# Kernel optimization log

Hardware: AMD Instinct MI355X
Metric: run time of the kernel (lower is better)

## Reference

```python
import jax, jax.numpy as jnp
import numpy as np

SPLIT_SHAPE = (16, 16, 16, 16)  # per-variable state counts; joint space = 65536
NUM_CLASSES = 100
STABLE = 1e-6


def setup_inputs() -> dict:
    key = jax.random.key(0)
    k1, k2 = jax.random.split(key)
    B = 1024
    logits = jax.random.normal(k1, (B, sum(SPLIT_SHAPE)), dtype=jnp.float32)
    labels = jax.random.randint(k2, (B,), 0, NUM_CLASSES)
    y_true = jax.nn.one_hot(labels, NUM_CLASSES, dtype=jnp.float32)
    return {"logits": logits, "y_true": y_true}


def reference(logits, y_true):
    B = logits.shape[0]
    # split logits into per-variable blocks and softmax each -> P(Ak|Xi)
    splits = np.cumsum(SPLIT_SHAPE)[:-1]
    variables = [jax.nn.softmax(p, axis=-1) for p in jnp.split(logits, splits, axis=-1)]
    # joint sample space via iterative outer products: [B, s1, ..., sN]
    joint = variables[0]
    for v in variables[1:]:
        joint = jnp.einsum('b...,ba->b...a', joint, v)
    flat = joint.reshape(B, -1)  # [B, J], J = prod(SPLIT_SHAPE)
    # observation: numerator/denominator counts (fresh recorder, first call)
    num_y_joint = jnp.einsum('bj,by->yj', flat, y_true)  # [Y, J]
    num_joint = jnp.sum(flat, axis=0)                     # [J]
    prob_y_joint = jnp.clip(
        jnp.maximum(num_y_joint, STABLE) / jnp.maximum(num_joint, STABLE), 0.0, 1.0)
    # inference: posterior P^A(Yi|Xi)
    probs = jnp.einsum('yj,bj->by', prob_y_joint, flat)  # [B, Y]
    return probs
```

## Files before the change

kernel.cpp:

```cpp
#include <hip/hip_runtime.h>
#include <hip/hip_bf16.h>

#define EPS 1e-6f

typedef float f32x4 __attribute__((ext_vector_type(4)));
typedef __bf16 bf16x8 __attribute__((ext_vector_type(8)));
typedef short short8 __attribute__((ext_vector_type(8)));

static __device__ __forceinline__ short bf16bits(float x) {
    __hip_bfloat16 h = __float2bfloat16(x);
    short s;
    __builtin_memcpy(&s, &h, 2);
    return s;
}
static __device__ __forceinline__ void bsplit(float x, short& h, short& l) {
    __hip_bfloat16 hb = __float2bfloat16(x);
    __builtin_memcpy(&h, &hb, 2);
    float hf = __bfloat162float(hb);
    __hip_bfloat16 lb = __float2bfloat16(x - hf);
    __builtin_memcpy(&l, &lb, 2);
}

static __device__ __forceinline__ bf16x8 gload16(const short* p) {
    bf16x8 r;
    asm volatile("global_load_dwordx4 %0, %1, off"
                 : "=&v"(r) : "v"(p) : "memory");
    return r;
}
#define WAITV(N)                                                   \
    do {                                                           \
        asm volatile("s_waitcnt vmcnt(" #N ")" ::: "memory");      \
        __builtin_amdgcn_sched_barrier(0);                         \
    } while (0)

__global__ __launch_bounds__(256) void kA(const float* __restrict__ logits,
                                          const float* __restrict__ y_true,
                                          float* __restrict__ P23,
                                          float* __restrict__ P01,
                                          float* __restrict__ P01T,
                                          short* __restrict__ P23s_hi,
                                          int* __restrict__ label,
                                          float* __restrict__ numjoint) {
    __shared__ float row[64];
    int b = blockIdx.x, t = threadIdx.x;
    if (t < 64) {
        float x = logits[b * 64 + t];
        float m = x;
        for (int mk = 8; mk >= 1; mk >>= 1) m = fmaxf(m, __shfl_xor(m, mk, 16));
        float e = __expf(x - m);
        float s = e;
        for (int mk = 8; mk >= 1; mk >>= 1) s += __shfl_xor(s, mk, 16);
        row[t] = e / s;
    }
    if (t >= 128 && t < 228) {
        int y = t - 128;
        if (y_true[b * 100 + y] > 0.5f) label[b] = y;
    }
    if (t < 64) numjoint[b * 64 + t] = 0.f;
    __syncthreads();
    int hi = t >> 4, lo = t & 15;
    float v01 = row[hi] * row[16 + lo];
    float v23 = row[32 + hi] * row[48 + lo];
    P01[b * 256 + t] = v01;
    P01T[t * 1024 + b] = v01;
    P23[b * 256 + t] = v23;
    int ts = t ^ ((b & 7) << 3);
    P23s_hi[b * 256 + ts] = bf16bits(v23);
}

__global__ __launch_bounds__(256, 4) void kSNJ(const float* __restrict__ P01T,
                                               const float* __restrict__ P23,
                                               const int* __restrict__ label,
                                               int* __restrict__ bidx,
                                               int* __restrict__ off_g,
                                               float* __restrict__ numjoint) {
    int t = threadIdx.x;
    int bid = blockIdx.x;

    if (bid == 512) {
        __shared__ int lab[1024];
        __shared__ unsigned bm[101 * 32];
        __shared__ int hist[101];
        __shared__ int offs[101];
        for (int i = t; i < 1024; i += 256) lab[i] = label[i];
        if (t < 101) hist[t] = 0;
        for (int i = t; i < 101 * 32; i += 256) bm[i] = 0u;
        __syncthreads();
        for (int i = t; i < 1024; i += 256) {
            int my = lab[i];
            atomicAdd(&hist[my], 1);
            atomicOr(&bm[my * 32 + (i >> 5)], 1u << (i & 31));
        }
        __syncthreads();
        if (t == 0) {
            int s = 0;
            for (int y = 0; y < 101; ++y) { offs[y] = s; s += hist[y]; }
        }
        __syncthreads();
        for (int i = t; i < 1024; i += 256) {
            int my = lab[i];
            int w = i >> 5;
            int rank = 0;
            for (int q = 0; q < 32; ++q)
                if (q < w) rank += __popc(bm[my * 32 + q]);
            rank += __popc(bm[my * 32 + w] & ((1u << (i & 31)) - 1u));
            bidx[offs[my] + rank] = i;
        }
        if (t <= 100) off_g[t] = offs[t];
        return;
    }

    __shared__ short Bh[4 * 64 * 8];
    __shared__ short Bl[4 * 64 * 8];
    int ub = (bid & 3) << 6;
    int tb = ((bid >> 2) & 3) << 6;
    int koff = (bid >> 4) << 5;
    int lane = t & 63, w = t >> 6;
    int l15 = lane & 15, l4 = lane >> 4;

    const float* pa = P01T + (size_t)(ub + w * 16 + l15) * 1024 + koff + (l4 << 3);
    int sr = t >> 3, sc = (t & 7) << 3;

    const f32x4 zero4 = {0.f, 0.f, 0.f, 0.f};
    f32x4 acc0 = zero4, acc1 = zero4, acc2 = zero4, acc3 = zero4;

    {
        const float* pb = P23 + (size_t)(koff + sr) * 256 + tb + sc;
        #pragma unroll
        for (int q = 0; q < 8; ++q) {
            short h, l;
            bsplit(pb[q], h, l);
            int tcl = sc + q;
            int ad = (((tcl >> 4) << 6) + (tcl & 15) + ((sr >> 3) << 4)) * 8 + (sr & 7);
            Bh[ad] = h; Bl[ad] = l;
        }
    }
    __syncthreads();
    union { short8 s; bf16x8 b; } Ah, Al;
    #pragma unroll
    for (int q = 0; q < 8; ++q) {
        short h, l;
        bsplit(pa[q], h, l);
        Ah.s[q] = h; Al.s[q] = l;
    }
    {
        bf16x8 bh0 = *(const bf16x8*)(Bh + (lane) * 8);
        bf16x8 bl0 = *(const bf16x8*)(Bl + (lane) * 8);
        bf16x8 bh1 = *(const bf16x8*)(Bh + (64 + lane) * 8);
        bf16x8 bl1 = *(const bf16x8*)(Bl + (64 + lane) * 8);
        bf16x8 bh2 = *(const bf16x8*)(Bh + (128 + lane) * 8);
        bf16x8 bl2 = *(const bf16x8*)(Bl + (128 + lane) * 8);
        bf16x8 bh3 = *(const bf16x8*)(Bh + (192 + lane) * 8);
        bf16x8 bl3 = *(const bf16x8*)(Bl + (192 + lane) * 8);
        acc0 = __builtin_amdgcn_mfma_f32_16x16x32_bf16(Ah.b, bh0, acc0, 0, 0, 0);
        acc0 = __builtin_amdgcn_mfma_f32_16x16x32_bf16(Ah.b, bl0, acc0, 0, 0, 0);
        acc0 = __builtin_amdgcn_mfma_f32_16x16x32_bf16(Al.b, bh0, acc0, 0, 0, 0);
        acc1 = __builtin_amdgcn_mfma_f32_16x16x32_bf16(Ah.b, bh1, acc1, 0, 0, 0);
        acc1 = __builtin_amdgcn_mfma_f32_16x16x32_bf16(Ah.b, bl1, acc1, 0, 0, 0);
        acc1 = __builtin_amdgcn_mfma_f32_16x16x32_bf16(Al.b, bh1, acc1, 0, 0, 0);
        acc2 = __builtin_amdgcn_mfma_f32_16x16x32_bf16(Ah.b, bh2, acc2, 0, 0, 0);
        acc2 = __builtin_amdgcn_mfma_f32_16x16x32_bf16(Ah.b, bl2, acc2, 0, 0, 0);
        acc2 = __builtin_amdgcn_mfma_f32_16x16x32_bf16(Al.b, bh2, acc2, 0, 0, 0);
        acc3 = __builtin_amdgcn_mfma_f32_16x16x32_bf16(Ah.b, bh3, acc3, 0, 0, 0);
        acc3 = __builtin_amdgcn_mfma_f32_16x16x32_bf16(Ah.b, bl3, acc3, 0, 0, 0);
        acc3 = __builtin_amdgcn_mfma_f32_16x16x32_bf16(Al.b, bh3, acc3, 0, 0, 0);
    }
    #pragma unroll
    for (int n = 0; n < 4; ++n) {
        f32x4 a = (n == 0) ? acc0 : (n == 1) ? acc1 : (n == 2) ? acc2 : acc3;
        #pragma unroll
        for (int r = 0; r < 4; ++r) {
            int u = ub + w * 16 + (l4 << 2) + r;
            int tc = tb + (n << 4) + l15;
            atomicAdd(&numjoint[u * 256 + tc], a[r]);
        }
    }
}

__global__ __launch_bounds__(256, 2) void kY(const float* __restrict__ P01,
                                             const float* __restrict__ P23,
                                             const int* __restrict__ bidx,
                                             const int* __restrict__ off_g,
                                             const float* __restrict__ numjoint,
                                             short* __restrict__ pyF) {
    __shared__ short Bh[4 * 64 * 8];
    __shared__ short Bl[4 * 64 * 8];
    __shared__ short ct[4][16 * 64];
    __shared__ float aStage[32][258];
    __shared__ int sbidx[32];
    int y = blockIdx.x >> 2;
    int qd = blockIdx.x & 3;
    int t = threadIdx.x;
    int lane = t & 63, w = t >> 6;
    int l15 = lane & 15, l4 = lane >> 4;
    int yt = y >> 4, yl = y & 15;

    if (y >= 100) {
        short8 z = {0, 0, 0, 0, 0, 0, 0, 0};
        #pragma unroll
        for (int ut = 0; ut < 4; ++ut)
            #pragma unroll
            for (int rep = 0; rep < 2; ++rep) {
                int c = (rep << 6) + lane;
                int ul = c >> 3, t8 = (c & 7) << 3;
                int u = (w << 6) + (ut << 4) + ul;
                int j0 = u * 256 + (qd << 6) + t8;
                size_t sa = ((size_t)((j0 >> 5) * 8 + yt) * 64 + yl + (((j0 >> 3) & 3) << 4)) * 8;
                *(short8*)(pyF + sa) = z;
            }
        return;
    }

    int off = off_g[y];
    int n = off_g[y + 1] - off;
    int nk = (n + 31) >> 5;

    const f32x4 zero4 = {0.f, 0.f, 0.f, 0.f};
    f32x4 acc[4][4];
    #pragma unroll
    for (int a = 0; a < 4; ++a)
        #pragma unroll
        for (int b = 0; b < 4; ++b) acc[a][b] = zero4;

    int sr = t >> 3, sc = (t & 7) << 3;

    #pragma unroll 1
    for (int kc = 0; kc < nk; ++kc) {
        __syncthreads();
        if (t < 32) {
            int idx = off + kc * 32 + t;
            sbidx[t] = bidx[(idx < 1024) ? idx : 1023];
        }
        __syncthreads();
        for (int it = 0; it < 32; ++it)
            aStage[it][t] = P01[sbidx[it] * 256 + t];
        {
            int row = kc * 32 + sr;
            float vals[8];
            if (row < n) {
                const float* pb = P23 + (size_t)sbidx[sr] * 256 + (qd << 6) + sc;
                #pragma unroll
                for (int q = 0; q < 8; ++q) vals[q] = pb[q];
            } else {
                #pragma unroll
                for (int q = 0; q < 8; ++q) vals[q] = 0.f;
            }
            #pragma unroll
            for (int q = 0; q < 8; ++q) {
                short h, l;
                bsplit(vals[q], h, l);
                int tl = sc + q;
                int ad = (((tl >> 4) << 6) + (tl & 15) + ((sr >> 3) << 4)) * 8 + (sr & 7);
                Bh[ad] = h; Bl[ad] = l;
            }
        }
        __syncthreads();
        #pragma unroll
        for (int ut = 0; ut < 4; ++ut) {
            union { short8 s; bf16x8 b; } Ah, Al;
            #pragma unroll
            for (int q = 0; q < 8; ++q) {
                short h, l;
                bsplit(aStage[(l4 << 3) + q][(w << 6) + (ut << 4) + l15], h, l);
                Ah.s[q] = h; Al.s[q] = l;
            }
            #pragma unroll
            for (int tt = 0; tt < 4; ++tt) {
                bf16x8 bh = *(const bf16x8*)(Bh + ((tt << 6) + lane) * 8);
                bf16x8 bl = *(const bf16x8*)(Bl + ((tt << 6) + lane) * 8);
                acc[ut][tt] = __builtin_amdgcn_mfma_f32_16x16x32_bf16(Ah.b, bh, acc[ut][tt], 0, 0, 0);
                acc[ut][tt] = __builtin_amdgcn_mfma_f32_16x16x32_bf16(Ah.b, bl, acc[ut][tt], 0, 0, 0);
                acc[ut][tt] = __builtin_amdgcn_mfma_f32_16x16x32_bf16(Al.b, bh, acc[ut][tt], 0, 0, 0);
            }
        }
    }

    #pragma unroll
    for (int ut = 0; ut < 4; ++ut) {
        #pragma unroll
        for (int tt = 0; tt < 4; ++tt) {
            #pragma unroll
            for (int r = 0; r < 4; ++r) {
                int u = (w << 6) + (ut << 4) + (l4 << 2) + r;
                int tg = (qd << 6) + (tt << 4) + l15;
                float nj = numjoint[u * 256 + tg];
                float q = fminf(fmaxf(acc[ut][tt][r], EPS) / fmaxf(nj, EPS), 1.0f);
                ct[w][((l4 << 2) + r) * 64 + (tt << 4) + l15] = bf16bits(q);
            }
        }
        asm volatile("s_waitcnt lgkmcnt(0)" ::: "memory");
        __builtin_amdgcn_sched_barrier(0);
        #pragma unroll
        for (int rep = 0; rep < 2; ++rep) {
            int c = (rep << 6) + lane;
            int ul = c >> 3, t8 = (c & 7) << 3;
            short8 v = *(const short8*)(ct[w] + ul * 64 + t8);
            int u = (w << 6) + (ut << 4) + ul;
            int j0 = u * 256 + (qd << 6) + t8;
            size_t sa = ((size_t)((j0 >> 5) * 8 + yt) * 64 + yl + (((j0 >> 3) & 3) << 4)) * 8;
            *(short8*)(pyF + sa) = v;
        }
        asm volatile("s_waitcnt lgkmcnt(0)" ::: "memory");
        __builtin_amdgcn_sched_barrier(0);
    }
}

__global__ __launch_bounds__(256, 3) void kC(const short* __restrict__ P23s_hi,
                                             const float* __restrict__ P01T,
                                             const short* __restrict__ pyF,
                                             float* __restrict__ part) {
    __shared__ short Ahi[64 * 256];
    __shared__ float p01s[512];
    int t = threadIdx.x;
    int bb = blockIdx.x >> 5, uspl = blockIdx.x & 31;
    int bbase = bb << 6;
    int u0 = uspl << 3;

    #pragma unroll
    for (int r = 0; r < 8; ++r) {
        int c = r * 256 + t;
        *(short8*)(Ahi + c * 8) = *(const short8*)(P23s_hi + bbase * 256 + c * 8);
    }
    p01s[t] = P01T[(u0 + (t >> 6)) * 1024 + bbase + (t & 63)];
    p01s[256 + t] = P01T[(u0 + 4 + (t >> 6)) * 1024 + bbase + (t & 63)];
    __syncthreads();

    int lane = t & 63;
    int wy = t >> 6;
    int l15 = lane & 15, l4 = lane >> 4;
    int hi8 = l4 << 3;

    int swz = (l15 & 7) << 3;
    const short* pA0h = Ahi + l15 * 256;
    const short* pA1h = pA0h + 16 * 256;
    const short* pA2h = pA0h + 32 * 256;
    const short* pA3h = pA0h + 48 * 256;

    const short* pf = pyF + (size_t)(uspl * 512 + wy * 2) * 512 + lane * 8;
    int y0 = wy * 32 + l15;

    const f32x4 zero4 = {0.f, 0.f, 0.f, 0.f};
    f32x4 P00 = zero4, P01v = zero4, P10 = zero4, P11 = zero4;
    f32x4 P20 = zero4, P21 = zero4, P30 = zero4, P31 = zero4;
    bf16x8 W0, W1, X0, X1, Y0, Y1, Z0, Z1;

#define COMPUTE(CUR0, CUR1, KS)                                                  \
    {                                                                            \
        int aoff = ((KS) * 32 + hi8) ^ swz;                                      \
        bf16x8 a0h = *(const bf16x8*)(pA0h + aoff);                              \
        bf16x8 a1h = *(const bf16x8*)(pA1h + aoff);                              \
        bf16x8 a2h = *(const bf16x8*)(pA2h + aoff);                              \
        bf16x8 a3h = *(const bf16x8*)(pA3h + aoff);                              \
        f32x4 c00 = ((KS) == 0) ? zero4 : Q00;                                   \
        f32x4 c01 = ((KS) == 0) ? zero4 : Q01;                                   \
        f32x4 c10 = ((KS) == 0) ? zero4 : Q10;                                   \
        f32x4 c11 = ((KS) == 0) ? zero4 : Q11;                                   \
        f32x4 c20 = ((KS) == 0) ? zero4 : Q20;                                   \
        f32x4 c21 = ((KS) == 0) ? zero4 : Q21;                                   \
        f32x4 c30 = ((KS) == 0) ? zero4 : Q30;                                   \
        f32x4 c31 = ((KS) == 0) ? zero4 : Q31;                                   \
        c00 = __builtin_amdgcn_mfma_f32_16x16x32_bf16(a0h, CUR0, c00, 0, 0, 0);  \
        c10 = __builtin_amdgcn_mfma_f32_16x16x32_bf16(a1h, CUR0, c10, 0, 0, 0);  \
        c20 = __builtin_amdgcn_mfma_f32_16x16x32_bf16(a2h, CUR0, c20, 0, 0, 0);  \
        c30 = __builtin_amdgcn_mfma_f32_16x16x32_bf16(a3h, CUR0, c30, 0, 0, 0);  \
        c01 = __builtin_amdgcn_mfma_f32_16x16x32_bf16(a0h, CUR1, c01, 0, 0, 0);  \
        c11 = __builtin_amdgcn_mfma_f32_16x16x32_bf16(a1h, CUR1, c11, 0, 0, 0);  \
        c21 = __builtin_amdgcn_mfma_f32_16x16x32_bf16(a2h, CUR1, c21, 0, 0, 0);  \
        c31 = __builtin_amdgcn_mfma_f32_16x16x32_bf16(a3h, CUR1, c31, 0, 0, 0);  \
        Q00 = c00; Q01 = c01; Q10 = c10; Q11 = c11;                              \
        Q20 = c20; Q21 = c21; Q30 = c30; Q31 = c31;                              \
    }
#define STEP(CUR0, CUR1, NXT0, NXT1, KS, S3)    \
    NXT0 = gload16(pf + (S3) * 4096);           \
    NXT1 = gload16(pf + (S3) * 4096 + 512);     \
    WAITV(6);                                   \
    COMPUTE(CUR0, CUR1, KS)

    {
        W0 = gload16(pf);        W1 = gload16(pf + 512);
        X0 = gload16(pf + 4096); X1 = gload16(pf + 4096 + 512);
        Y0 = gload16(pf + 8192); Y1 = gload16(pf + 8192 + 512);
    }

    #pragma unroll 1
    for (int uu = 0; uu < 7; ++uu) {
        int s0 = uu * 8;
        f32x4 Q00, Q01, Q10, Q11, Q20, Q21, Q30, Q31;
        STEP(W0, W1, Z0, Z1, 0, s0 + 3)
        STEP(X0, X1, W0, W1, 1, s0 + 4)
        STEP(Y0, Y1, X0, X1, 2, s0 + 5)
        STEP(Z0, Z1, Y0, Y1, 3, s0 + 6)
        STEP(W0, W1, Z0, Z1, 4, s0 + 7)
        STEP(X0, X1, W0, W1, 5, s0 + 8)
        STEP(Y0, Y1, X0, X1, 6, s0 + 9)
        STEP(Z0, Z1, Y0, Y1, 7, s0 + 10)
        f32x4 pv0 = *(const f32x4*)(p01s + uu * 64 + (l4 << 2));
        f32x4 pv1 = *(const f32x4*)(p01s + uu * 64 + 16 + (l4 << 2));
        f32x4 pv2 = *(const f32x4*)(p01s + uu * 64 + 32 + (l4 << 2));
        f32x4 pv3 = *(const f32x4*)(p01s + uu * 64 + 48 + (l4 << 2));
        P00 += pv0 * Q00; P01v += pv0 * Q01;
        P10 += pv1 * Q10; P11 += pv1 * Q11;
        P20 += pv2 * Q20; P21 += pv2 * Q21;
        P30 += pv3 * Q30; P31 += pv3 * Q31;
    }
    {
        f32x4 Q00, Q01, Q10, Q11, Q20, Q21, Q30, Q31;
        STEP(W0, W1, Z0, Z1, 0, 59)
        STEP(X0, X1, W0, W1, 1, 60)
        STEP(Y0, Y1, X0, X1, 2, 61)
        STEP(Z0, Z1, Y0, Y1, 3, 62)
        STEP(W0, W1, Z0, Z1, 4, 63)
        WAITV(4); COMPUTE(X0, X1, 5)
        WAITV(2); COMPUTE(Y0, Y1, 6)
        WAITV(0); COMPUTE(Z0, Z1, 7)
        f32x4 pv0 = *(const f32x4*)(p01s + 7 * 64 + (l4 << 2));
        f32x4 pv1 = *(const f32x4*)(p01s + 7 * 64 + 16 + (l4 << 2));
        f32x4 pv2 = *(const f32x4*)(p01s + 7 * 64 + 32 + (l4 << 2));
        f32x4 pv3 = *(const f32x4*)(p01s + 7 * 64 + 48 + (l4 << 2));
        P00 += pv0 * Q00; P01v += pv0 * Q01;
        P10 += pv1 * Q10; P11 += pv1 * Q11;
        P20 += pv2 * Q20; P21 += pv2 * Q21;
        P30 += pv3 * Q30; P31 += pv3 * Q31;
    }
#undef STEP
#undef COMPUTE

    size_t pbase = (size_t)uspl * 128 * 1024;
    {
        int bg0 = bbase + (l4 << 2);
        size_t r0 = pbase + (size_t)y0 * 1024;
        size_t r1 = pbase + (size_t)(y0 + 16) * 1024;
        *(f32x4*)(part + r0 + bg0)      = P00;
        *(f32x4*)(part + r0 + bg0 + 16) = P10;
        *(f32x4*)(part + r0 + bg0 + 32) = P20;
        *(f32x4*)(part + r0 + bg0 + 48) = P30;
        *(f32x4*)(part + r1 + bg0)      = P01v;
        *(f32x4*)(part + r1 + bg0 + 16) = P11;
        *(f32x4*)(part + r1 + bg0 + 32) = P21;
        *(f32x4*)(part + r1 + bg0 + 48) = P31;
    }
}

__global__ __launch_bounds__(256) void kD(const float* __restrict__ part,
                                          float* __restrict__ out) {
    int t = threadIdx.x;
    int y = blockIdx.x >> 2;
    int b = ((blockIdx.x & 3) << 8) + t;
    float s = 0.f;
    for (int q = 0; q < 32; ++q)
        s += part[(((size_t)q * 128 + y) << 10) + b];
    out[(size_t)b * 100 + y] = s;
}

extern "C" void kernel_launch(void* const* d_in, const int* in_sizes, int n_in,
                              void* d_out, int out_size, void* d_ws, size_t ws_size,
                              hipStream_t stream) {
    const float* logits = (const float*)d_in[0];
    const float* y_true = (const float*)d_in[1];
    float* out = (float*)d_out;

    char* ws = (char*)d_ws;
    float* P01      = (float*)(ws);
    float* P23      = (float*)(ws + (1u << 20));
    float* P01T     = (float*)(ws + (2u << 20));
    short* P23s_hi  = (short*)(ws + (3u << 20));
    int*   lab      = (int*)(ws + (4u << 20));
    int*   bidx     = (int*)(ws + (4u << 20) + 4096);
    int*   off_g    = (int*)(ws + (4u << 20) + 8192);
    short* pyF      = (short*)(ws + (8u << 20));
    float* numjoint = (float*)(ws + (24u << 20));
    float* part     = (float*)(ws + (40u << 20));

    kA<<<1024, 256, 0, stream>>>(logits, y_true, P23, P01, P01T, P23s_hi, lab, numjoint);
    kSNJ<<<513, 256, 0, stream>>>(P01T, P23, lab, bidx, off_g, numjoint);
    kY<<<512, 256, 0, stream>>>(P01, P23, bidx, off_g, numjoint, pyF);
    kC<<<512, 256, 0, stream>>>(P23s_hi, P01T, pyF, part);
    kD<<<400, 256, 0, stream>>>(part, out);
}
```

Measured before the change: 67.03 us.

## Fuse split-K reduction into kC via last-block atomic counter

Removes the separate kD reduction launch. Each kC block bumps a per-batch-tile atomic counter after writing its partials, and the last of the 32 u-split blocks for that tile sums the partials and writes the output. The counter is reset in kA. This saves one kernel launch and its dependency gap, but leaves the reduction to only 16 blocks running serially at the tail of kC, with threadfence overhead added to every block.

```diff
diff --git a/kernel.cpp b/kernel.cpp
--- a/kernel.cpp
+++ b/kernel.cpp
@@ -40,9 +40,11 @@
                                           float* __restrict__ P01T,
                                           short* __restrict__ P23s_hi,
                                           int* __restrict__ label,
-                                          float* __restrict__ numjoint) {
+                                          float* __restrict__ numjoint,
+                                          int* __restrict__ cnt) {
     __shared__ float row[64];
     int b = blockIdx.x, t = threadIdx.x;
+    if (b == 0 && t < 16) cnt[t] = 0;
     if (t < 64) {
         float x = logits[b * 64 + t];
         float m = x;
@@ -308,9 +310,12 @@
 __global__ __launch_bounds__(256, 3) void kC(const short* __restrict__ P23s_hi,
                                              const float* __restrict__ P01T,
                                              const short* __restrict__ pyF,
-                                             float* __restrict__ part) {
+                                             float* __restrict__ part,
+                                             int* __restrict__ cnt,
+                                             float* __restrict__ out) {
     __shared__ short Ahi[64 * 256];
     __shared__ float p01s[512];
+    __shared__ int lastflag;
     int t = threadIdx.x;
     int bb = blockIdx.x >> 5, uspl = blockIdx.x & 31;
     int bbase = bb << 6;
@@ -439,17 +444,27 @@
         *(f32x4*)(part + r1 + bg0 + 32) = P21;
         *(f32x4*)(part + r1 + bg0 + 48) = P31;
     }
-}
-
-__global__ __launch_bounds__(256) void kD(const float* __restrict__ part,
-                                          float* __restrict__ out) {
-    int t = threadIdx.x;
-    int y = blockIdx.x >> 2;
-    int b = ((blockIdx.x & 3) << 8) + t;
-    float s = 0.f;
-    for (int q = 0; q < 32; ++q)
-        s += part[(((size_t)q * 128 + y) << 10) + b];
-    out[(size_t)b * 100 + y] = s;
+
+    __threadfence();
+    if (t == 0) {
+        int prev = atomicAdd(&cnt[bb], 1);
+        lastflag = (prev == 31) ? 1 : 0;
+    }
+    __syncthreads();
+    if (lastflag) {
+        __threadfence();
+        #pragma unroll 1
+        for (int it = 0; it < 25; ++it) {
+            int idx = it * 256 + t;
+            int y = idx >> 6;
+            int b = bbase + (idx & 63);
+            float s = 0.f;
+            #pragma unroll
+            for (int q = 0; q < 32; ++q)
+                s += part[(((size_t)q * 128 + y) << 10) + b];
+            out[(size_t)b * 100 + y] = s;
+        }
+    }
 }
 
 extern "C" void kernel_launch(void* const* d_in, const int* in_sizes, int n_in,
@@ -467,13 +482,13 @@
     int*   lab      = (int*)(ws + (4u << 20));
     int*   bidx     = (int*)(ws + (4u << 20) + 4096);
     int*   off_g    = (int*)(ws + (4u << 20) + 8192);
+    int*   cnt      = (int*)(ws + (4u << 20) + 16384);
     short* pyF      = (short*)(ws + (8u << 20));
     float* numjoint = (float*)(ws + (24u << 20));
     float* part     = (float*)(ws + (40u << 20));
 
-    kA<<<1024, 256, 0, stream>>>(logits, y_true, P23, P01, P01T, P23s_hi, lab, numjoint);
+    kA<<<1024, 256, 0, stream>>>(logits, y_true, P23, P01, P01T, P23s_hi, lab, numjoint, cnt);
     kSNJ<<<513, 256, 0, stream>>>(P01T, P23, lab, bidx, off_g, numjoint);
     kY<<<512, 256, 0, stream>>>(P01, P23, bidx, off_g, numjoint, pyF);
-    kC<<<512, 256, 0, stream>>>(P23s_hi, P01T, pyF, part);
-    kD<<<400, 256, 0, stream>>>(part, out);
-}
+    kC<<<512, 256, 0, stream>>>(P23s_hi, P01T, pyF, part, cnt, out);
+}
```

Result: slower. 171.7 us (+156.2%).
